# Kernel optimization log

Hardware: AMD Instinct MI355X
Metric: run time of the kernel (lower is better)

## Reference

```python
import jax, jax.numpy as jnp
import numpy as np

B, T, D, U, R = 64, 512, 256, 256, 4


def setup_inputs() -> dict:
    key = jax.random.key(0)
    ks = jax.random.split(key, 12)
    inputs = jax.random.normal(ks[0], (B, T, D), dtype=jnp.float32)
    # per-timestep dependency indices into past timesteps; must satisfy dep[t] <= t
    dependencies = jnp.minimum(
        jax.random.randint(ks[1], (T, R - 1), 0, T), jnp.arange(T)[:, None]
    ).astype(jnp.int32)
    mask = jax.random.randint(ks[2], (B, T), 0, 2).astype(jnp.int32)
    initial_states = jax.random.normal(ks[3], (R, B, U), dtype=jnp.float32) * 0.1
    s = 1.0 / np.sqrt(U)
    def w(k, shape):
        return jax.random.normal(k, shape, dtype=jnp.float32) * s
    return dict(
        inputs=inputs, dependencies=dependencies, mask=mask, initial_states=initial_states,
        Wz=w(ks[4], (D, U)), Wr=w(ks[5], (D, U)), Wh=w(ks[6], (D, U)),
        Uz=w(ks[7], (U, U)), Ur=w(ks[8], (U, U)), Uh=w(ks[9], (U, U)),
        bz=jnp.zeros((U,), jnp.float32), br=jnp.zeros((U,), jnp.float32), bh=jnp.zeros((U,), jnp.float32),
    )


def reference(inputs, dependencies, mask, initial_states, Wz, Wr, Wh, Uz, Ur, Uh, bz, br, bh):
    Bn, Tn, _ = inputs.shape
    Rn = initial_states.shape[0]
    Un = Uz.shape[0]

    x = jnp.swapaxes(inputs, 0, 1)              # [T, B, D]  (time_major swap)
    m = jnp.swapaxes(mask, 0, 1).astype(bool)   # [T, B]
    # dependencies[i] is consumed AFTER step i (sets states for step i+1) -> shift by one
    dep_in = jnp.concatenate(
        [jnp.zeros((1, dependencies.shape[1]), dependencies.dtype), dependencies[:-1]], axis=0
    )

    def cell(x_t, states):
        # states: [R, B, U]  (child-sum Graph-GRU over recurrent_size predecessor states)
        r = jax.nn.sigmoid(x_t @ Wr + states @ Ur + br)          # [R, B, U]
        h_sum = states.sum(0)                                    # [B, U]
        z = jax.nn.sigmoid(x_t @ Wz + h_sum @ Uz + bz)
        h_tilde = jnp.tanh(x_t @ Wh + (r * states).sum(0) @ Uh + bh)
        h = z * (h_sum / Rn) + (1.0 - z) * h_tilde
        return h  # GRU: output == new state

    def step(carry, xs):
        prev_out, prev_state, buf, t = carry
        x_t, m_t, dep_t = xs
        gathered = buf[dep_t]                                    # [R-1, B, U] irregular history gather
        cand = jnp.concatenate([prev_state[None], gathered], axis=0)
        states = jnp.where(t == 0, initial_states, cand)
        h = cell(x_t, states)
        mt = m_t[:, None]                                        # [B, 1]
        out_m = jnp.where(mt, h, prev_out)                       # masked output (pre_output carry)
        st_m = jnp.where(mt, h, prev_state)                      # masked state  (pre_states carry)
        buf = buf.at[t].set(st_m)                                # successive_states[t]
        return (out_m, st_m, buf, t + 1), out_m

    carry0 = (
        jnp.zeros((Bn, Un), inputs.dtype),
        jnp.zeros((Bn, Un), inputs.dtype),
        jnp.zeros((Tn, Bn, Un), inputs.dtype),
        jnp.array(0, jnp.int32),
    )
    (last_out, last_state, _, _), outs = jax.lax.scan(step, carry0, (x, m, dep_in))

    # zero_output_for_mask
    last_out = jnp.where(m[-1][:, None], last_out, jnp.zeros_like(last_out))
    outs = jnp.where(m[:, :, None], outs, jnp.zeros_like(outs))
    outputs = jnp.swapaxes(outs, 0, 1)                           # back to [B, T, U]
    return outputs, last_out, last_state
```

## Files before the change

### kernel.cpp

```cpp
#include <hip/hip_runtime.h>
#include <cstdint>
#include <cstddef>

#define BN 64
#define TN 512
#define DN 256
#define UN 256
#define NC 768
#define SLOTS (TN + 5)
#define ZSLOT (TN + 4)
#define WL 6

__device__ __forceinline__ float sigm(float x) {
  return 1.0f / (1.0f + __expf(-x));
}
__device__ __forceinline__ float tanh_fast(float x) {
  float e = __expf(-2.0f * x);
  return 2.0f / (1.0f + e) - 1.0f;
}

__global__ __launch_bounds__(256) void build_wcat(
    const float* __restrict__ Wr, const float* __restrict__ Wz, const float* __restrict__ Wh,
    const float* __restrict__ br, const float* __restrict__ bz, const float* __restrict__ bh,
    float* __restrict__ wcat, float* __restrict__ bias)
{
  int idx = blockIdx.x * 256 + threadIdx.x;
  if (idx < DN * NC) {
    int k = idx / NC, c = idx % NC;
    float v;
    if (c < 256)      v = Wr[k * UN + c];
    else if (c < 512) v = Wz[k * UN + (c - 256)];
    else              v = Wh[k * UN + (c - 512)];
    wcat[idx] = v;
  }
  if (idx < NC) {
    bias[idx] = (idx < 256) ? br[idx] : ((idx < 512) ? bz[idx - 256] : bh[idx - 512]);
  }
}

__global__ __launch_bounds__(256) void gemm_xw(
    const float* __restrict__ X, const float* __restrict__ Wc,
    const float* __restrict__ bias, float* __restrict__ P)
{
  __shared__ float As[32][68];
  __shared__ float Bs[32][64];
  const int tid = threadIdx.x;
  const int m0 = blockIdx.x * 64;
  const int n0 = blockIdx.y * 64;
  const int ty = tid >> 4, tx = tid & 15;
  float acc[4][4] = {};

  const int ar = tid >> 3;
  const int ak = (tid & 7) * 4;
  const int bk = tid >> 4;
  const int bn = (tid & 15) * 4;

  for (int k0 = 0; k0 < DN; k0 += 32) {
    float4 a0 = *(const float4*)(X + (size_t)(m0 + ar) * DN + k0 + ak);
    float4 a1 = *(const float4*)(X + (size_t)(m0 + 32 + ar) * DN + k0 + ak);
    As[ak + 0][ar] = a0.x; As[ak + 1][ar] = a0.y; As[ak + 2][ar] = a0.z; As[ak + 3][ar] = a0.w;
    As[ak + 0][32 + ar] = a1.x; As[ak + 1][32 + ar] = a1.y; As[ak + 2][32 + ar] = a1.z; As[ak + 3][32 + ar] = a1.w;
    *(float4*)&Bs[bk][bn]      = *(const float4*)(Wc + (size_t)(k0 + bk) * NC + n0 + bn);
    *(float4*)&Bs[bk + 16][bn] = *(const float4*)(Wc + (size_t)(k0 + bk + 16) * NC + n0 + bn);
    __syncthreads();
#pragma unroll
    for (int kk = 0; kk < 32; kk++) {
      float4 av = *(const float4*)&As[kk][ty * 4];
      float4 bv = *(const float4*)&Bs[kk][tx * 4];
      acc[0][0] += av.x * bv.x; acc[0][1] += av.x * bv.y; acc[0][2] += av.x * bv.z; acc[0][3] += av.x * bv.w;
      acc[1][0] += av.y * bv.x; acc[1][1] += av.y * bv.y; acc[1][2] += av.y * bv.z; acc[1][3] += av.y * bv.w;
      acc[2][0] += av.z * bv.x; acc[2][1] += av.z * bv.y; acc[2][2] += av.z * bv.z; acc[2][3] += av.z * bv.w;
      acc[3][0] += av.w * bv.x; acc[3][1] += av.w * bv.y; acc[3][2] += av.w * bv.z; acc[3][3] += av.w * bv.w;
    }
    __syncthreads();
  }
  float4 bb = *(const float4*)(bias + n0 + tx * 4);
#pragma unroll
  for (int i = 0; i < 4; i++) {
    float4 o;
    o.x = acc[i][0] + bb.x; o.y = acc[i][1] + bb.y;
    o.z = acc[i][2] + bb.z; o.w = acc[i][3] + bb.w;
    *(float4*)(P + (size_t)(m0 + ty * 4 + i) * NC + n0 + tx * 4) = o;
  }
}

__global__ __launch_bounds__(1024, 4) void recurrent_kernel(
    const float* __restrict__ P,
    const float* __restrict__ Ur, const float* __restrict__ Uz, const float* __restrict__ Uh,
    const int* __restrict__ dep, const int* __restrict__ mask,
    const float* __restrict__ init,
    float* __restrict__ out,
    float* __restrict__ buf_s, float* __restrict__ buf_pr, float* __restrict__ buf_pz)
{
  const int b = blockIdx.x;
  const int tid = threadIdx.x;
  const int g = tid >> 8;
  const int u = tid & 255;
  const int wv = tid >> 6;
  const int mat = wv & 1;
  const int s   = wv >> 1;
  const int l   = tid & 63;

  float wh[64];
  {
    const float* p2 = Uh + (size_t)(64 * g) * UN + u;
#pragma unroll
    for (int kk = 0; kk < 64; kk++) {
      wh[kk] = p2[(size_t)kk * UN];
    }
  }
  const float* Um = mat ? Uz : Ur;

  __shared__ float4 wlds[2][8][WL][64];
  __shared__ float ls[4][256], lpr[4][256], lpz[4][256];
  __shared__ float lx[NC];
  __shared__ float rs[256], hs[256], zv[256], hv[256];
  __shared__ float red0[4][256];
  __shared__ float redd[2][8][256];
  __shared__ float scur[256], prcur[256], pzcur[256];
  __shared__ int eff[TN], nxt[TN + 1];
  __shared__ int mloc[TN];
  __shared__ int deploc[TN * 3];

  for (int i = tid; i < 2 * 8 * WL * 64; i += 1024) {
    int mm = i / (8 * WL * 64);
    int r2 = i % (8 * WL * 64);
    int ss = r2 / (WL * 64);
    int rr = (r2 / 64) % WL;
    int ll = i & 63;
    wlds[mm][ss][rr][ll] = ((const float4*)(mm ? Uz : Ur))[(size_t)(32 * ss + rr) * 64 + ll];
  }
  for (int i = tid; i < TN; i += 1024) mloc[i] = mask[b * TN + i];
  for (int i = tid; i < TN * 3; i += 1024) deploc[i] = dep[i];

  const size_t bufBase = (size_t)b * SLOTS * UN;

  {
    float v = init[((size_t)g * BN + b) * UN + u];
    ls[g][u] = v;
    buf_s[bufBase + (size_t)(TN + g) * UN + u] = v;
    if (tid < 256) {
      scur[u] = 0.0f; prcur[u] = 0.0f; pzcur[u] = 0.0f;
      buf_s[bufBase + (size_t)ZSLOT * UN + u] = 0.0f;
      buf_pr[bufBase + (size_t)ZSLOT * UN + u] = 0.0f;
      buf_pz[bufBase + (size_t)ZSLOT * UN + u] = 0.0f;
    }
  }
  __syncthreads();

  if (tid == 0) {
    int e = ZSLOT;
    for (int t2 = 0; t2 < TN; t2++) { if (mloc[t2]) e = t2; eff[t2] = e; }
  } else if (tid == 64) {
    nxt[TN] = TN;
    int e = TN;
    for (int t2 = TN - 1; t2 >= 0; t2--) { if (mloc[t2]) e = t2; nxt[t2] = e; }
  }

  auto projD = [&](const float* hsrc) {
    const float* hb = hsrc + 32 * s;
    float4 a = {0, 0, 0, 0};
#pragma unroll
    for (int r = 0; r < WL; r++) {
      float hk = hb[r];
      float4 w = wlds[mat][s][r][l];
      a.x = fmaf(hk, w.x, a.x); a.y = fmaf(hk, w.y, a.y);
      a.z = fmaf(hk, w.z, a.z); a.w = fmaf(hk, w.w, a.w);
    }
    const float4* p = (const float4*)Um + (size_t)(32 * s + WL) * 64 + l;
#pragma unroll 4
    for (int r = 0; r < 32 - WL; r++) {
      float hk = hb[WL + r];
      float4 w = p[(size_t)r * 64];
      a.x = fmaf(hk, w.x, a.x); a.y = fmaf(hk, w.y, a.y);
      a.z = fmaf(hk, w.z, a.z); a.w = fmaf(hk, w.w, a.w);
    }
    *(float4*)&redd[mat][s][4 * l] = a;
  };

#pragma unroll 1
  for (int gg = 0; gg < 4; gg++) {
    projD(&ls[gg][0]);
    __syncthreads();
    if (tid < 256) {
      float prn = 0.0f, pzn = 0.0f;
#pragma unroll
      for (int q = 0; q < 8; q++) { prn += redd[0][q][tid]; pzn += redd[1][q][tid]; }
      buf_pr[bufBase + (size_t)(TN + gg) * UN + tid] = prn;
      buf_pz[bufBase + (size_t)(TN + gg) * UN + tid] = pzn;
    }
    __syncthreads();
  }

  const size_t outB = (size_t)b * TN * UN;
  const size_t pB = (size_t)b * TN * NC;

  {
    int t0 = nxt[0];
    if (t0 < TN && tid < NC) lx[tid] = P[pB + (size_t)t0 * NC + tid];
  }
  __syncthreads();

#pragma unroll 1
  for (int t = 0; t < TN; t++) {
    if (mloc[t] == 0) {
      if (tid < 256) out[outB + (size_t)t * UN + u] = 0.0f;
      continue;
    }
    if (t > 0 && g == 0) {
      ls[0][u] = scur[u]; lpr[0][u] = prcur[u]; lpz[0][u] = pzcur[u];
    } else {
      int src = (t == 0) ? (TN + g) : eff[deploc[(t - 1) * 3 + (g - 1)]];
      size_t base = bufBase + (size_t)src * UN + u;
      ls[g][u]  = buf_s[base];
      lpr[g][u] = buf_pr[base];
      lpz[g][u] = buf_pz[base];
    }
    __syncthreads();
    if (tid < 256) {
      float s0 = ls[0][u], s1 = ls[1][u], s2 = ls[2][u], s3 = ls[3][u];
      float xr = lx[u];
      float r0 = sigm(xr + lpr[0][u]);
      float r1 = sigm(xr + lpr[1][u]);
      float r2 = sigm(xr + lpr[2][u]);
      float r3 = sigm(xr + lpr[3][u]);
      rs[u] = r0 * s0 + r1 * s1 + r2 * s2 + r3 * s3;
      hs[u] = (s0 + s1) + (s2 + s3);
      zv[u] = sigm(lx[256 + u] + ((lpz[0][u] + lpz[1][u]) + (lpz[2][u] + lpz[3][u])));
    }
    __syncthreads();
    {
      float a0 = 0, a1 = 0, a2 = 0, a3 = 0;
      const float4* v4 = (const float4*)&rs[64 * g];
#pragma unroll
      for (int kk = 0; kk < 16; kk++) {
        float4 v = v4[kk];
        a0 += v.x * wh[4 * kk];     a1 += v.y * wh[4 * kk + 1];
        a2 += v.z * wh[4 * kk + 2]; a3 += v.w * wh[4 * kk + 3];
      }
      red0[g][u] = (a0 + a1) + (a2 + a3);
    }
    __syncthreads();
    if (tid < 256) {
      float ht = tanh_fast(lx[512 + u] + ((red0[0][u] + red0[1][u]) + (red0[2][u] + red0[3][u])));
      float z = zv[u];
      float h = z * hs[u] * 0.25f + (1.0f - z) * ht;
      hv[u] = h; scur[u] = h;
      out[outB + (size_t)t * UN + u] = h;
    }
    __syncthreads();
    {
      const int tn = nxt[t + 1];
      if (tn < TN && tid < NC) lx[tid] = P[pB + (size_t)tn * NC + tid];
    }
    projD(hv);
    __syncthreads();
    if (tid < 256) {
      float prn = 0.0f, pzn = 0.0f;
#pragma unroll
      for (int q = 0; q < 8; q++) { prn += redd[0][q][tid]; pzn += redd[1][q][tid]; }
      prcur[tid] = prn; pzcur[tid] = pzn;
      size_t base = bufBase + (size_t)t * UN + tid;
      buf_s[base]  = hv[tid];
      buf_pr[base] = prn;
      buf_pz[base] = pzn;
    }
    __syncthreads();
  }

  if (tid < 256) {
    float lst = scur[u];
    out[(size_t)BN * TN * UN + (size_t)b * UN + u] = mloc[TN - 1] ? lst : 0.0f;
    out[(size_t)BN * TN * UN + (size_t)BN * UN + (size_t)b * UN + u] = lst;
  }
}

extern "C" void kernel_launch(void* const* d_in, const int* in_sizes, int n_in,
                              void* d_out, int out_size, void* d_ws, size_t ws_size,
                              hipStream_t stream) {
  const float* inputs       = (const float*)d_in[0];
  const int*   dependencies = (const int*)d_in[1];
  const int*   mask         = (const int*)d_in[2];
  const float* initial      = (const float*)d_in[3];
  const float* Wz = (const float*)d_in[4];
  const float* Wr = (const float*)d_in[5];
  const float* Wh = (const float*)d_in[6];
  const float* Uz = (const float*)d_in[7];
  const float* Ur = (const float*)d_in[8];
  const float* Uh = (const float*)d_in[9];
  const float* bz = (const float*)d_in[10];
  const float* br = (const float*)d_in[11];
  const float* bh = (const float*)d_in[12];

  float* out = (float*)d_out;
  float* ws  = (float*)d_ws;
  float* wcat    = ws;
  float* bias    = wcat + (size_t)DN * NC;
  float* precomp = bias + NC;
  float* buf_s   = precomp + (size_t)BN * TN * NC;
  float* buf_pr  = buf_s + (size_t)BN * SLOTS * UN;
  float* buf_pz  = buf_pr + (size_t)BN * SLOTS * UN;

  build_wcat<<<(DN * NC + 255) / 256, 256, 0, stream>>>(Wr, Wz, Wh, br, bz, bh, wcat, bias);
  gemm_xw<<<dim3(BN * TN / 64, NC / 64), 256, 0, stream>>>(inputs, wcat, bias, precomp);
  recurrent_kernel<<<BN, 1024, 0, stream>>>(precomp, Ur, Uz, Uh, dependencies, mask, initial,
                                            out, buf_s, buf_pr, buf_pz);
}
```

Measured before the change: 1.838 ms.

## Prefetch next step's dependency states during projection and forward the current state

The irregular history gather for the next active timestep now runs alongside the hidden-state projection, writing into shared staging buffers. When a dependency points at the step just computed, the value is taken directly from the current-state registers and shared arrays instead of the global buffer. The gather-then-barrier phase at the top of each step is gone, and so is the trailing barrier. This is meant to hide global-memory gather latency inside the serial recurrence. The cost is extra shared-memory traffic, more reliance on subtle ordering between steps that can skip masked timesteps, and wider conditional logic per thread.

```diff
diff --git a/kernel.cpp b/kernel.cpp
--- a/kernel.cpp
+++ b/kernel.cpp
@@ -201,32 +201,57 @@
   }
   __syncthreads();
 
+  bool havePre = false;
+  int tprev = -1;
+
 #pragma unroll 1
   for (int t = 0; t < TN; t++) {
     if (mloc[t] == 0) {
       if (tid < 256) out[outB + (size_t)t * UN + u] = 0.0f;
       continue;
     }
-    if (t > 0 && g == 0) {
-      ls[0][u] = scur[u]; lpr[0][u] = prcur[u]; lpz[0][u] = pzcur[u];
-    } else {
-      int src = (t == 0) ? (TN + g) : eff[deploc[(t - 1) * 3 + (g - 1)]];
-      size_t base = bufBase + (size_t)src * UN + u;
-      ls[g][u]  = buf_s[base];
-      lpr[g][u] = buf_pr[base];
-      lpz[g][u] = buf_pz[base];
-    }
-    __syncthreads();
-    if (tid < 256) {
-      float s0 = ls[0][u], s1 = ls[1][u], s2 = ls[2][u], s3 = ls[3][u];
-      float xr = lx[u];
-      float r0 = sigm(xr + lpr[0][u]);
-      float r1 = sigm(xr + lpr[1][u]);
-      float r2 = sigm(xr + lpr[2][u]);
-      float r3 = sigm(xr + lpr[3][u]);
+    if (tid < 256) {
+      float xr = lx[u], xz = lx[256 + u];
+      float s0, p0, q0, s1, p1, q1, s2, p2, q2, s3, p3, q3;
+      if (havePre) {
+        s0 = scur[u]; p0 = prcur[u]; q0 = pzcur[u];
+        int d1 = eff[deploc[(t - 1) * 3 + 0]];
+        int d2 = eff[deploc[(t - 1) * 3 + 1]];
+        int d3 = eff[deploc[(t - 1) * 3 + 2]];
+        s1 = (d1 == tprev) ? scur[u] : ls[1][u];
+        p1 = (d1 == tprev) ? prcur[u] : lpr[1][u];
+        q1 = (d1 == tprev) ? pzcur[u] : lpz[1][u];
+        s2 = (d2 == tprev) ? scur[u] : ls[2][u];
+        p2 = (d2 == tprev) ? prcur[u] : lpr[2][u];
+        q2 = (d2 == tprev) ? pzcur[u] : lpz[2][u];
+        s3 = (d3 == tprev) ? scur[u] : ls[3][u];
+        p3 = (d3 == tprev) ? prcur[u] : lpr[3][u];
+        q3 = (d3 == tprev) ? pzcur[u] : lpz[3][u];
+      } else if (t == 0) {
+        size_t b0 = bufBase + (size_t)(TN + 0) * UN + u;
+        size_t b1 = bufBase + (size_t)(TN + 1) * UN + u;
+        size_t b2 = bufBase + (size_t)(TN + 2) * UN + u;
+        size_t b3 = bufBase + (size_t)(TN + 3) * UN + u;
+        s0 = buf_s[b0]; p0 = buf_pr[b0]; q0 = buf_pz[b0];
+        s1 = buf_s[b1]; p1 = buf_pr[b1]; q1 = buf_pz[b1];
+        s2 = buf_s[b2]; p2 = buf_pr[b2]; q2 = buf_pz[b2];
+        s3 = buf_s[b3]; p3 = buf_pr[b3]; q3 = buf_pz[b3];
+      } else {
+        s0 = scur[u]; p0 = prcur[u]; q0 = pzcur[u];
+        size_t b1 = bufBase + (size_t)eff[deploc[(t - 1) * 3 + 0]] * UN + u;
+        size_t b2 = bufBase + (size_t)eff[deploc[(t - 1) * 3 + 1]] * UN + u;
+        size_t b3 = bufBase + (size_t)eff[deploc[(t - 1) * 3 + 2]] * UN + u;
+        s1 = buf_s[b1]; p1 = buf_pr[b1]; q1 = buf_pz[b1];
+        s2 = buf_s[b2]; p2 = buf_pr[b2]; q2 = buf_pz[b2];
+        s3 = buf_s[b3]; p3 = buf_pr[b3]; q3 = buf_pz[b3];
+      }
+      float r0 = sigm(xr + p0);
+      float r1 = sigm(xr + p1);
+      float r2 = sigm(xr + p2);
+      float r3 = sigm(xr + p3);
       rs[u] = r0 * s0 + r1 * s1 + r2 * s2 + r3 * s3;
       hs[u] = (s0 + s1) + (s2 + s3);
-      zv[u] = sigm(lx[256 + u] + ((lpz[0][u] + lpz[1][u]) + (lpz[2][u] + lpz[3][u])));
+      zv[u] = sigm(xz + ((q0 + q1) + (q2 + q3)));
     }
     __syncthreads();
     {
@@ -251,7 +276,19 @@
     __syncthreads();
     {
       const int tn = nxt[t + 1];
-      if (tn < TN && tid < NC) lx[tid] = P[pB + (size_t)tn * NC + tid];
+      if (tn < TN) {
+        if (tid < NC) lx[tid] = P[pB + (size_t)tn * NC + tid];
+        if (tid < 768) {
+          int gi = tid >> 8;
+          int srcp = eff[deploc[(tn - 1) * 3 + gi]];
+          if (srcp != t) {
+            size_t base = bufBase + (size_t)srcp * UN + u;
+            ls[gi + 1][u]  = buf_s[base];
+            lpr[gi + 1][u] = buf_pr[base];
+            lpz[gi + 1][u] = buf_pz[base];
+          }
+        }
+      }
     }
     projD(hv);
     __syncthreads();
@@ -265,7 +302,8 @@
       buf_pr[base] = prn;
       buf_pz[base] = pzn;
     }
-    __syncthreads();
+    tprev = t;
+    havePre = true;
   }
 
   if (tid < 256) {
```

After: 2.084 ms. 1.13x slower.

## Enlarge input-projection GEMM tiles to 128x128 and double-buffer shared memory

Applied to the files above, without the earlier changes.

Rewrites the precompute GEMM to use 128x128 output tiles with an 8x8 per-thread register tile and a two-stage shared memory buffer over K=16 slices. The aim is higher arithmetic intensity per shared-memory load and overlapping the next tile's load with compute. It raises register use and shared memory per block and reduces block count, which can lower occupancy. The recurrent kernel, which likely dominates runtime, is untouched.

```diff
diff --git a/kernel.cpp b/kernel.cpp
--- a/kernel.cpp
+++ b/kernel.cpp
@@ -10,6 +10,11 @@
 #define SLOTS (TN + 5)
 #define ZSLOT (TN + 4)
 #define WL 6
+
+#define GBM 128
+#define GBN 128
+#define GBK 16
+#define APAD 132
 
 __device__ __forceinline__ float sigm(float x) {
   return 1.0f / (1.0f + __expf(-x));
@@ -38,49 +43,81 @@
   }
 }
 
+#define FMA4(ar_, av_, bv_)                      \
+  ar_[0] = fmaf(av_, bv_.x, ar_[0]);             \
+  ar_[1] = fmaf(av_, bv_.y, ar_[1]);             \
+  ar_[2] = fmaf(av_, bv_.z, ar_[2]);             \
+  ar_[3] = fmaf(av_, bv_.w, ar_[3]);
+
 __global__ __launch_bounds__(256) void gemm_xw(
     const float* __restrict__ X, const float* __restrict__ Wc,
     const float* __restrict__ bias, float* __restrict__ P)
 {
-  __shared__ float As[32][68];
-  __shared__ float Bs[32][64];
+  __shared__ float As[2][GBK][APAD];
+  __shared__ float Bs[2][GBK][GBN];
   const int tid = threadIdx.x;
-  const int m0 = blockIdx.x * 64;
-  const int n0 = blockIdx.y * 64;
-  const int ty = tid >> 4, tx = tid & 15;
-  float acc[4][4] = {};
-
-  const int ar = tid >> 3;
-  const int ak = (tid & 7) * 4;
-  const int bk = tid >> 4;
-  const int bn = (tid & 15) * 4;
-
-  for (int k0 = 0; k0 < DN; k0 += 32) {
+  const int m0 = blockIdx.x * GBM;
+  const int n0 = blockIdx.y * GBN;
+  const int tx = tid & 15;
+  const int ty = tid >> 4;
+
+  const int ar = tid >> 2;
+  const int ak = (tid & 3) * 4;
+  const int bk = tid >> 5;
+  const int bn = (tid & 31) * 4;
+
+  float acc[2][2][4][4] = {};
+
+  auto stage = [&](int k0, int buf) {
     float4 a0 = *(const float4*)(X + (size_t)(m0 + ar) * DN + k0 + ak);
-    float4 a1 = *(const float4*)(X + (size_t)(m0 + 32 + ar) * DN + k0 + ak);
-    As[ak + 0][ar] = a0.x; As[ak + 1][ar] = a0.y; As[ak + 2][ar] = a0.z; As[ak + 3][ar] = a0.w;
-    As[ak + 0][32 + ar] = a1.x; As[ak + 1][32 + ar] = a1.y; As[ak + 2][32 + ar] = a1.z; As[ak + 3][32 + ar] = a1.w;
-    *(float4*)&Bs[bk][bn]      = *(const float4*)(Wc + (size_t)(k0 + bk) * NC + n0 + bn);
-    *(float4*)&Bs[bk + 16][bn] = *(const float4*)(Wc + (size_t)(k0 + bk + 16) * NC + n0 + bn);
-    __syncthreads();
-#pragma unroll
-    for (int kk = 0; kk < 32; kk++) {
-      float4 av = *(const float4*)&As[kk][ty * 4];
-      float4 bv = *(const float4*)&Bs[kk][tx * 4];
-      acc[0][0] += av.x * bv.x; acc[0][1] += av.x * bv.y; acc[0][2] += av.x * bv.z; acc[0][3] += av.x * bv.w;
-      acc[1][0] += av.y * bv.x; acc[1][1] += av.y * bv.y; acc[1][2] += av.y * bv.z; acc[1][3] += av.y * bv.w;
-      acc[2][0] += av.z * bv.x; acc[2][1] += av.z * bv.y; acc[2][2] += av.z * bv.z; acc[2][3] += av.z * bv.w;
-      acc[3][0] += av.w * bv.x; acc[3][1] += av.w * bv.y; acc[3][2] += av.w * bv.z; acc[3][3] += av.w * bv.w;
-    }
-    __syncthreads();
-  }
-  float4 bb = *(const float4*)(bias + n0 + tx * 4);
-#pragma unroll
-  for (int i = 0; i < 4; i++) {
-    float4 o;
-    o.x = acc[i][0] + bb.x; o.y = acc[i][1] + bb.y;
-    o.z = acc[i][2] + bb.z; o.w = acc[i][3] + bb.w;
-    *(float4*)(P + (size_t)(m0 + ty * 4 + i) * NC + n0 + tx * 4) = o;
+    float4 a1 = *(const float4*)(X + (size_t)(m0 + 64 + ar) * DN + k0 + ak);
+    As[buf][ak + 0][ar] = a0.x; As[buf][ak + 1][ar] = a0.y;
+    As[buf][ak + 2][ar] = a0.z; As[buf][ak + 3][ar] = a0.w;
+    As[buf][ak + 0][64 + ar] = a1.x; As[buf][ak + 1][64 + ar] = a1.y;
+    As[buf][ak + 2][64 + ar] = a1.z; As[buf][ak + 3][64 + ar] = a1.w;
+    *(float4*)&Bs[buf][bk][bn]     = *(const float4*)(Wc + (size_t)(k0 + bk) * NC + n0 + bn);
+    *(float4*)&Bs[buf][bk + 8][bn] = *(const float4*)(Wc + (size_t)(k0 + bk + 8) * NC + n0 + bn);
+  };
+
+  stage(0, 0);
+  __syncthreads();
+#pragma unroll 1
+  for (int kt = 0; kt < DN / GBK; kt++) {
+    const int buf = kt & 1;
+    if (kt + 1 < DN / GBK) stage((kt + 1) * GBK, buf ^ 1);
+#pragma unroll
+    for (int kk = 0; kk < GBK; kk++) {
+      float4 a0 = *(const float4*)&As[buf][kk][ty * 4];
+      float4 a1 = *(const float4*)&As[buf][kk][64 + ty * 4];
+      float4 b0 = *(const float4*)&Bs[buf][kk][tx * 4];
+      float4 b1 = *(const float4*)&Bs[buf][kk][64 + tx * 4];
+      FMA4(acc[0][0][0], a0.x, b0); FMA4(acc[0][0][1], a0.y, b0);
+      FMA4(acc[0][0][2], a0.z, b0); FMA4(acc[0][0][3], a0.w, b0);
+      FMA4(acc[0][1][0], a0.x, b1); FMA4(acc[0][1][1], a0.y, b1);
+      FMA4(acc[0][1][2], a0.z, b1); FMA4(acc[0][1][3], a0.w, b1);
+      FMA4(acc[1][0][0], a1.x, b0); FMA4(acc[1][0][1], a1.y, b0);
+      FMA4(acc[1][0][2], a1.z, b0); FMA4(acc[1][0][3], a1.w, b0);
+      FMA4(acc[1][1][0], a1.x, b1); FMA4(acc[1][1][1], a1.y, b1);
+      FMA4(acc[1][1][2], a1.z, b1); FMA4(acc[1][1][3], a1.w, b1);
+    }
+    __syncthreads();
+  }
+
+  float4 bb0 = *(const float4*)(bias + n0 + tx * 4);
+  float4 bb1 = *(const float4*)(bias + n0 + 64 + tx * 4);
+#pragma unroll
+  for (int mi = 0; mi < 2; mi++) {
+#pragma unroll
+    for (int i = 0; i < 4; i++) {
+      const size_t row = (size_t)(m0 + mi * 64 + ty * 4 + i) * NC + n0;
+      float4 o0, o1;
+      o0.x = acc[mi][0][i][0] + bb0.x; o0.y = acc[mi][0][i][1] + bb0.y;
+      o0.z = acc[mi][0][i][2] + bb0.z; o0.w = acc[mi][0][i][3] + bb0.w;
+      o1.x = acc[mi][1][i][0] + bb1.x; o1.y = acc[mi][1][i][1] + bb1.y;
+      o1.z = acc[mi][1][i][2] + bb1.z; o1.w = acc[mi][1][i][3] + bb1.w;
+      *(float4*)(P + row + tx * 4) = o0;
+      *(float4*)(P + row + 64 + tx * 4) = o1;
+    }
   }
 }
 
@@ -302,7 +339,7 @@
   float* buf_pz  = buf_pr + (size_t)BN * SLOTS * UN;
 
   build_wcat<<<(DN * NC + 255) / 256, 256, 0, stream>>>(Wr, Wz, Wh, br, bz, bh, wcat, bias);
-  gemm_xw<<<dim3(BN * TN / 64, NC / 64), 256, 0, stream>>>(inputs, wcat, bias, precomp);
+  gemm_xw<<<dim3(BN * TN / GBM, NC / GBN), 256, 0, stream>>>(inputs, wcat, bias, precomp);
   recurrent_kernel<<<BN, 1024, 0, stream>>>(precomp, Ur, Uz, Uh, dependencies, mask, initial,
                                             out, buf_s, buf_pr, buf_pz);
 }
```

After: 1.823 ms. No clear change (-0.8%).
